# Kernel optimization log

Measured on AMD Instinct MI355X. Metric: run time of the kernel, lower is better.

## Reference

```python
import jax, jax.numpy as jnp
import numpy as np
import math

B, T, D, H = 2, 2048, 1024, 16
DH = D // H          # 64
NB = DH // 2         # 32 rotary pairs
EPS = 1e-5


def setup_inputs() -> dict:
    key = jax.random.key(0)
    ks = jax.random.split(key, 20)
    x = jax.random.normal(ks[0], (B, T, D), dtype=jnp.float32)
    angles = jax.random.uniform(ks[1], (B, H, T, NB), dtype=jnp.float32) * (2.0 * math.pi)
    cos_a = jnp.cos(angles)
    sin_a = jnp.sin(angles)
    sigma = jax.random.uniform(ks[2], (B, T, H, NB), dtype=jnp.float32)
    causal_mask = jnp.triu(jnp.ones((T, T), dtype=bool), k=1)  # True above diag -> masked
    w = lambda k, i, o: jax.random.normal(k, (i, o), dtype=jnp.float32) * 0.02
    return {
        "x": x, "cos_a": cos_a, "sin_a": sin_a, "sigma": sigma, "causal_mask": causal_mask,
        "ln1_g": jnp.ones((D,), jnp.float32), "ln1_b": jnp.zeros((D,), jnp.float32),
        "wq": w(ks[3], D, D), "bq": jnp.zeros((D,), jnp.float32),
        "wk": w(ks[4], D, D), "bk": jnp.zeros((D,), jnp.float32),
        "wv": w(ks[5], D, D), "bv": jnp.zeros((D,), jnp.float32),
        "wo": w(ks[6], D, D), "bo": jnp.zeros((D,), jnp.float32),
        "ln2_g": jnp.ones((D,), jnp.float32), "ln2_b": jnp.zeros((D,), jnp.float32),
        "w1": w(ks[7], D, 4 * D), "b1": jnp.zeros((4 * D,), jnp.float32),
        "w2": w(ks[8], 4 * D, D), "b2": jnp.zeros((D,), jnp.float32),
    }


def _layer_norm(x, g, b):
    mu = jnp.mean(x, axis=-1, keepdims=True)
    var = jnp.mean(jnp.square(x - mu), axis=-1, keepdims=True)
    return (x - mu) * jax.lax.rsqrt(var + EPS) * g + b


def _apply_rope(q, cos_a, sin_a):
    # q: (B,H,T,DH); rotate even/odd pairs by per-pair angles (B,H,T,NB)
    q1 = q[..., 0::2]
    q2 = q[..., 1::2]
    re = q1 * cos_a - q2 * sin_a
    im = q1 * sin_a + q2 * cos_a
    return jnp.stack([re, im], axis=-1).reshape(q.shape)


def reference(x, cos_a, sin_a, sigma, causal_mask,
              ln1_g, ln1_b, wq, bq, wk, bk, wv, bv, wo, bo,
              ln2_g, ln2_b, w1, b1, w2, b2):
    h = _layer_norm(x, ln1_g, ln1_b)
    Q = (h @ wq + bq).reshape(B, T, H, DH).transpose(0, 2, 1, 3)
    K = (h @ wk + bk).reshape(B, T, H, DH).transpose(0, 2, 1, 3)
    V = (h @ wv + bv).reshape(B, T, H, DH).transpose(0, 2, 1, 3)
    Q = _apply_rope(Q, cos_a, sin_a)
    K = _apply_rope(K, cos_a, sin_a)
    # per-(B,H,T) temperature from mean uncertainty
    temp = 1.0 + jnp.mean(sigma, axis=-1).transpose(0, 2, 1)  # (B,H,T)
    scale = math.sqrt(DH)
    scores = jnp.einsum("bhtd,bhsd->bhts", Q, K) / (scale * temp[..., None])
    scores = jnp.where(causal_mask[None, None], -jnp.inf, scores)
    attn = jax.nn.softmax(scores, axis=-1)
    out = jnp.einsum("bhts,bhsd->bhtd", attn, V)
    out = out.transpose(0, 2, 1, 3).reshape(B, T, D)
    x = x + (out @ wo + bo)
    h2 = _layer_norm(x, ln2_g, ln2_b)
    ffn = jax.nn.gelu(h2 @ w1 + b1, approximate=False) @ w2 + b2
    return x + ffn
```

## Files before the change

kernel.cpp:

```cpp
#include <hip/hip_runtime.h>

typedef unsigned short ushort;
typedef unsigned int uint;

typedef __attribute__((ext_vector_type(8))) short short8;
typedef __attribute__((ext_vector_type(8))) unsigned short ushort8;
typedef __attribute__((ext_vector_type(4))) unsigned short ushort4v;
typedef __attribute__((ext_vector_type(4))) float f32x4;
typedef __attribute__((ext_vector_type(4))) uint uint4v;

#define DEV static __device__ __forceinline__

DEV ushort f2b(float f){
  union { float f; uint u; } v; v.f = f;
  uint u = v.u;
  u += 0x7fffu + ((u >> 16) & 1u);
  return (ushort)(u >> 16);
}
DEV float b2f(ushort h){
  union { uint u; float f; } v; v.u = ((uint)h) << 16;
  return v.f;
}
DEV uint cvt_pk_bf16(float lo, float hi){
  uint r;
  asm("v_cvt_pk_bf16_f32 %0, %1, %2" : "=v"(r) : "v"(lo), "v"(hi));
  return r;
}
DEV ushort f2b1(float f){ return (ushort)cvt_pk_bf16(f, f); }
DEV float exp2v(float x){
  float r;
  asm("v_exp_f32 %0, %1" : "=v"(r) : "v"(x));
  return r;
}
DEV float gelu_f(float x){
  float z = fabsf(x) * 0.70710678118654752f;
  float t = __builtin_amdgcn_rcpf(1.f + 0.3275911f * z);
  float poly = t * (0.254829592f + t * (-0.284496736f + t * (1.421413741f +
               t * (-1.453152027f + t * 1.061405429f))));
  float e = exp2v(-z * z * 1.44269504088896f);
  float erf_abs = 1.f - poly * e;
  float erf_s = copysignf(erf_abs, x);
  return 0.5f * x * (1.f + erf_s);
}

constexpr int Bc = 2, Tc = 2048, Dc = 1024, Hc = 16, DHc = 64, NBc = 32;
constexpr int Rc = Bc * Tc;
constexpr int D4c = 4 * Dc;

__global__ __launch_bounds__(256) void k_transcvt(const float* __restrict__ in,
                                                  ushort* __restrict__ out, int K, int N){
  __shared__ float tile[32][33];
  int n0 = blockIdx.x * 32, k0 = blockIdx.y * 32;
  int c = threadIdx.x & 31, r0 = threadIdx.x >> 5;
#pragma unroll
  for (int i = 0; i < 4; i++){
    int k = r0 + i * 8;
    tile[k][c] = in[(size_t)(k0 + k) * N + n0 + c];
  }
  __syncthreads();
#pragma unroll
  for (int i = 0; i < 4; i++){
    int n = r0 + i * 8;
    out[(size_t)(n0 + n) * K + k0 + c] = f2b(tile[c][n]);
  }
}

__global__ __launch_bounds__(256) void k_ln(const float* __restrict__ x, const float* __restrict__ g,
                                            const float* __restrict__ bb, ushort* __restrict__ out){
  int row = blockIdx.x, tid = threadIdx.x;
  const f32x4* xr = (const f32x4*)(x + (size_t)row * Dc);
  f32x4 v = xr[tid];
  float s  = v.x + v.y + v.z + v.w;
  float ss = v.x*v.x + v.y*v.y + v.z*v.z + v.w*v.w;
#pragma unroll
  for (int off = 32; off > 0; off >>= 1){
    s  += __shfl_xor(s,  off, 64);
    ss += __shfl_xor(ss, off, 64);
  }
  __shared__ float red[2][4];
  int w = tid >> 6;
  if ((tid & 63) == 0){ red[0][w] = s; red[1][w] = ss; }
  __syncthreads();
  s  = red[0][0] + red[0][1] + red[0][2] + red[0][3];
  ss = red[1][0] + red[1][1] + red[1][2] + red[1][3];
  float mu  = s * (1.f / Dc);
  float var = ss * (1.f / Dc) - mu * mu;
  float rs  = rsqrtf(var + 1e-5f);
  f32x4 gv = ((const f32x4*)g)[tid];
  f32x4 bv = ((const f32x4*)bb)[tid];
  ushort4v o;
  o.x = f2b((v.x - mu) * rs * gv.x + bv.x);
  o.y = f2b((v.y - mu) * rs * gv.y + bv.y);
  o.z = f2b((v.z - mu) * rs * gv.z + bv.z);
  o.w = f2b((v.w - mu) * rs * gv.w + bv.w);
  ((ushort4v*)(out + (size_t)row * Dc))[tid] = o;
}

#define GLDS(src, dst) __builtin_amdgcn_global_load_lds( \
    (const __attribute__((address_space(1))) void*)(src), \
    (__attribute__((address_space(3))) void*)(dst), 16, 0, 0)

#define STAGE128(nb_, k0_) do { \
  _Pragma("unroll") \
  for (int i_ = 0; i_ < 4; i_++){ \
    int chunk_ = w * 4 + i_; \
    GLDS(A  + (size_t)(m0 + chunk_ * 8 + rloc) * K + (k0_) + gsrc * 8, &SM[nb_][0][chunk_ * 512]); \
    GLDS(Bt + (size_t)(n0 + chunk_ * 8 + rloc) * K + (k0_) + gsrc * 8, &SM[nb_][1][chunk_ * 512]); \
  } \
} while(0)

#define GEMM_CORE(cb_) do { \
  _Pragma("unroll") \
  for (int ks = 0; ks < 2; ks++){ \
    const int gs = (ks * 4 + lg) ^ l7; \
    short8 aF[4], bF[4]; \
    _Pragma("unroll") \
    for (int mi = 0; mi < 4; mi++) aF[mi] = *(const short8*)&SM[cb_][0][(arow + mi * 16) * 64 + gs * 8]; \
    _Pragma("unroll") \
    for (int ni = 0; ni < 4; ni++) bF[ni] = *(const short8*)&SM[cb_][1][(brow + ni * 16) * 64 + gs * 8]; \
    _Pragma("unroll") \
    for (int mi = 0; mi < 4; mi++) \
      _Pragma("unroll") \
      for (int ni = 0; ni < 4; ni++) \
        acc[mi][ni] = __builtin_amdgcn_mfma_f32_16x16x32_bf16(aF[mi], bF[ni], acc[mi][ni], 0, 0, 0); \
  } \
} while(0)

template<int OUT_BF16, int ACT_GELU, int HAS_RES>
__global__ __launch_bounds__(256) void k_gemm(const ushort* __restrict__ A, const ushort* __restrict__ Bt,
                                              const float* __restrict__ bias, const float* __restrict__ resid,
                                              void* __restrict__ Cout, int M, int N, int K){
  __shared__ ushort SM[2][2][8192];
  const int tid = threadIdx.x;
  const int m0 = blockIdx.y * 128, n0 = blockIdx.x * 128;
  const int w = tid >> 6, lane = tid & 63;
  const int wr = w >> 1, wc = w & 1;
  const int la15 = lane & 15, lg = lane >> 4, l7 = lane & 7;
  const int rloc = lane >> 3, gsrc = (lane & 7) ^ rloc;

  f32x4 acc[4][4];
#pragma unroll
  for (int i = 0; i < 4; i++)
#pragma unroll
    for (int j = 0; j < 4; j++) acc[i][j] = f32x4{0.f, 0.f, 0.f, 0.f};

  const int arow = wr * 64 + la15;
  const int brow = wc * 64 + la15;

  STAGE128(0, 0);
  __syncthreads();
  const int NT = K >> 6;
  for (int t = 0; t < NT; t++){
    const int cb = t & 1;
    if (t + 1 < NT) STAGE128(cb ^ 1, (t + 1) << 6);
    GEMM_CORE(cb);
    __syncthreads();
  }

  if (OUT_BF16){
    ushort* Cs = &SM[0][0][0];
#pragma unroll
    for (int mi = 0; mi < 4; mi++)
#pragma unroll
      for (int ni = 0; ni < 4; ni++){
        int ccl = wc * 64 + ni * 16 + la15;
        float bv = bias[n0 + ccl];
        f32x4 a4 = acc[mi][ni];
#pragma unroll
        for (int r = 0; r < 4; r++){
          int rl = wr * 64 + mi * 16 + lg * 4 + r;
          float v = a4[r] + bv;
          if (ACT_GELU) v = gelu_f(v);
          Cs[rl * 136 + ccl] = f2b1(v);
        }
      }
    __syncthreads();
#pragma unroll
    for (int p = 0; p < 8; p++){
      int row = p * 16 + (tid >> 4);
      int col = (tid & 15) * 8;
      ushort8 vv = *(const ushort8*)&Cs[row * 136 + col];
      *(ushort8*)((ushort*)Cout + (size_t)(m0 + row) * N + n0 + col) = vv;
    }
  } else {
#pragma unroll
    for (int mi = 0; mi < 4; mi++)
#pragma unroll
      for (int ni = 0; ni < 4; ni++){
        int cc = n0 + wc * 64 + ni * 16 + la15;
        float bv = bias[cc];
        f32x4 a4 = acc[mi][ni];
#pragma unroll
        for (int r = 0; r < 4; r++){
          int rr = m0 + wr * 64 + mi * 16 + lg * 4 + r;
          float v = a4[r] + bv;
          if (HAS_RES) v += resid[(size_t)rr * N + cc];
          ((float*)Cout)[(size_t)rr * N + cc] = v;
        }
      }
  }
}

__global__ __launch_bounds__(256) void k_gemm_qkv(const ushort* __restrict__ A, const ushort* __restrict__ Bt,
                                                  const float* __restrict__ bq_, const float* __restrict__ bk_,
                                                  const float* __restrict__ bv_, ushort* __restrict__ oq,
                                                  ushort* __restrict__ ok, ushort* __restrict__ ovt, int K){
  __shared__ ushort SM[2][2][8192];
  const int tid = threadIdx.x;
  const int m0 = blockIdx.y * 128, n0 = blockIdx.x * 128;
  const int w = tid >> 6, lane = tid & 63;
  const int wr = w >> 1, wc = w & 1;
  const int la15 = lane & 15, lg = lane >> 4, l7 = lane & 7;
  const int rloc = lane >> 3, gsrc = (lane & 7) ^ rloc;

  f32x4 acc[4][4];
#pragma unroll
  for (int i = 0; i < 4; i++)
#pragma unroll
    for (int j = 0; j < 4; j++) acc[i][j] = f32x4{0.f, 0.f, 0.f, 0.f};

  const int arow = wr * 64 + la15;
  const int brow = wc * 64 + la15;

  STAGE128(0, 0);
  __syncthreads();
  const int NT = K >> 6;
  for (int t = 0; t < NT; t++){
    const int cb = t & 1;
    if (t + 1 < NT) STAGE128(cb ^ 1, (t + 1) << 6);
    GEMM_CORE(cb);
    __syncthreads();
  }

  const int sel = n0 >> 10;
  ushort* Cs = &SM[0][0][0];
  if (sel < 2){
    const float* bias = sel == 0 ? bq_ : bk_;
    ushort* o = sel == 0 ? oq : ok;
#pragma unroll
    for (int mi = 0; mi < 4; mi++)
#pragma unroll
      for (int ni = 0; ni < 4; ni++){
        int ccl = wc * 64 + ni * 16 + la15;
        float bv = bias[(n0 & 1023) + ccl];
        f32x4 a4 = acc[mi][ni];
#pragma unroll
        for (int r = 0; r < 4; r++){
          int rl = wr * 64 + mi * 16 + lg * 4 + r;
          Cs[rl * 136 + ccl] = f2b1(a4[r] + bv);
        }
      }
    __syncthreads();
#pragma unroll
    for (int p = 0; p < 8; p++){
      int row = p * 16 + (tid >> 4);
      int col = (tid & 15) * 8;
      ushort8 vv = *(const ushort8*)&Cs[row * 136 + col];
      *(ushort8*)(o + (size_t)(m0 + row) * Dc + (n0 & 1023) + col) = vv;
    }
  } else {
#pragma unroll
    for (int mi = 0; mi < 4; mi++)
#pragma unroll
      for (int ni = 0; ni < 4; ni++){
        int ccl = wc * 64 + ni * 16 + la15;
        float bv = bv_[(n0 - 2048) + ccl];
        f32x4 a4 = acc[mi][ni];
#pragma unroll
        for (int r = 0; r < 4; r++){
          int rl = wr * 64 + mi * 16 + lg * 4 + r;
          Cs[ccl * 136 + rl] = f2b1(a4[r] + bv);
        }
      }
    __syncthreads();
    const int bb = m0 >> 11, t0 = m0 & 2047;
#pragma unroll
    for (int p = 0; p < 8; p++){
      int nl = p * 16 + (tid >> 4);
      int tl = (tid & 15) * 8;
      ushort8 vv = *(const ushort8*)&Cs[nl * 136 + tl];
      int ng = (n0 - 2048) + nl;
      *(ushort8*)(ovt + ((size_t)(bb * 1024 + ng) << 11) + t0 + tl) = vv;
    }
  }
}

__global__ __launch_bounds__(256) void k_rope(ushort* __restrict__ q, ushort* __restrict__ k,
                                              const float* __restrict__ ca, const float* __restrict__ sa){
  int idx = blockIdx.x * 256 + threadIdx.x;
  int nb = idx & 31;
  int hh = (idx >> 5) & 15;
  int t  = (idx >> 9) & 2047;
  int b  = idx >> 20;
  size_t base = (size_t)(b * Tc + t) * Dc + hh * DHc + nb * 2;
  int ai = ((b * Hc + hh) * Tc + t) * NBc + nb;
  float c = ca[ai], s = sa[ai];
  uint qu = *(const uint*)(q + base);
  float q1 = b2f((ushort)(qu & 0xffff)), q2 = b2f((ushort)(qu >> 16));
  *(uint*)(q + base) = cvt_pk_bf16(q1 * c - q2 * s, q1 * s + q2 * c);
  uint ku = *(const uint*)(k + base);
  float k1 = b2f((ushort)(ku & 0xffff)), k2 = b2f((ushort)(ku >> 16));
  *(uint*)(k + base) = cvt_pk_bf16(k1 * c - k2 * s, k1 * s + k2 * c);
}

__global__ __launch_bounds__(256) void k_iscale(const float* __restrict__ sigma, float* __restrict__ isc){
  int idx = blockIdx.x * 256 + threadIdx.x;
  int hh = idx & 15;
  int t  = (idx >> 4) & 2047;
  int b  = idx >> 15;
  const f32x4* sp = (const f32x4*)(sigma + (size_t)idx * NBc);
  float s = 0.f;
#pragma unroll
  for (int i = 0; i < 8; i++){ f32x4 v = sp[i]; s += v.x + v.y + v.z + v.w; }
  isc[(b * Hc + hh) * Tc + t] = 1.44269504088896f / (8.f * (1.f + s * (1.f / NBc)));
}

__global__ __launch_bounds__(64) void k_attn_mfma(const ushort* __restrict__ qb, const ushort* __restrict__ kb,
                                                  const ushort* __restrict__ vtb, const float* __restrict__ isc,
                                                  ushort* __restrict__ ao){
  __shared__ ushort smem[8192];
  const int bid = blockIdx.x;
  const int bh = bid & 31, b = bh >> 4, h = bh & 15;
  const int qt = 63 - (bid >> 5);
  const int lane = threadIdx.x;
  const int la15 = lane & 15, lg = lane >> 4, l7 = lane & 7;
  const int q0w = qt * 32;

  short8 qf[2][2];
  float iscv[2];
#pragma unroll
  for (int sub = 0; sub < 2; sub++){
    int qg = q0w + sub * 16 + la15;
    size_t rb = (size_t)(b * Tc + qg) * Dc + h * DHc;
    qf[sub][0] = *(const short8*)(qb + rb + lg * 8);
    qf[sub][1] = *(const short8*)(qb + rb + 32 + lg * 8);
    iscv[sub] = isc[bh * Tc + qg];
  }

  f32x4 O[2][4];
#pragma unroll
  for (int sub = 0; sub < 2; sub++)
#pragma unroll
    for (int dt = 0; dt < 4; dt++) O[sub][dt] = f32x4{0.f, 0.f, 0.f, 0.f};
  float lacc[2] = {0.f, 0.f};

  const ushort* kbase  = kb + (size_t)b * Tc * Dc + h * DHc;
  const ushort* vtbase = vtb + (size_t)bh * DHc * Tc;
  const int ktmax = q0w + 31;

  const int Rl = lane >> 3, sl = lane & 7;
  const int gK = sl ^ ((Rl & 3) ^ (((Rl >> 3) & 3) << 1));
  const int gV = sl ^ (Rl & 7);

#define STAGE_KV(kt_) do { \
  _Pragma("unroll") \
  for (int i_ = 0; i_ < 8; i_++){ \
    int R_ = i_ * 8 + Rl; \
    int gk_ = sl ^ ((R_ & 3) ^ (((R_ >> 3) & 3) << 1)); \
    GLDS(kbase + (size_t)((kt_) + R_) * Dc + gk_ * 8, &smem[i_ * 512]); \
    GLDS(vtbase + (size_t)R_ * Tc + (kt_) + gV * 8, &smem[4096 + i_ * 512]); \
  } \
} while(0)

#define COMPUTE_T(kt_) do { \
  _Pragma("unroll") \
  for (int sub = 0; sub < 2; sub++){ \
    f32x4 s_[4]; \
    __builtin_amdgcn_s_setprio(1); \
    _Pragma("unroll") \
    for (int t_ = 0; t_ < 4; t_++){ \
      s_[t_] = f32x4{0.f, 0.f, 0.f, 0.f}; \
      s_[t_] = __builtin_amdgcn_mfma_f32_16x16x32_bf16(kf[t_][0], qf[sub][0], s_[t_], 0, 0, 0); \
      s_[t_] = __builtin_amdgcn_mfma_f32_16x16x32_bf16(kf[t_][1], qf[sub][1], s_[t_], 0, 0, 0); \
    } \
    __builtin_amdgcn_s_setprio(0); \
    const int qg_ = q0w + sub * 16 + la15; \
    const float sc_ = iscv[sub]; \
    const bool diag_ = ((kt_) + 63 > q0w + sub * 16); \
    uint up_[4][2]; \
    float lp_ = 0.f; \
    _Pragma("unroll") \
    for (int t_ = 0; t_ < 4; t_++){ \
      _Pragma("unroll") \
      for (int pr_ = 0; pr_ < 2; pr_++){ \
        float e0_ = exp2v(s_[t_][2 * pr_] * sc_); \
        float e1_ = exp2v(s_[t_][2 * pr_ + 1] * sc_); \
        if (diag_){ \
          int kp0_ = (kt_) + ((t_ >> 1) << 5) + lg * 8 + ((t_ & 1) << 2) + 2 * pr_; \
          if (kp0_ > qg_)     e0_ = 0.f; \
          if (kp0_ + 1 > qg_) e1_ = 0.f; \
        } \
        lp_ += e0_ + e1_; \
        up_[t_][pr_] = cvt_pk_bf16(e0_, e1_); \
      } \
    } \
    lacc[sub] += lp_; \
    __builtin_amdgcn_s_setprio(1); \
    _Pragma("unroll") \
    for (int kh_ = 0; kh_ < 2; kh_++){ \
      union { uint4v w; short8 s8; } pfr_; \
      pfr_.w[0] = up_[kh_ * 2][0];     pfr_.w[1] = up_[kh_ * 2][1]; \
      pfr_.w[2] = up_[kh_ * 2 + 1][0]; pfr_.w[3] = up_[kh_ * 2 + 1][1]; \
      _Pragma("unroll") \
      for (int dt_ = 0; dt_ < 4; dt_++) \
        O[sub][dt_] = __builtin_amdgcn_mfma_f32_16x16x32_bf16(vtf[dt_][kh_], pfr_.s8, O[sub][dt_], 0, 0, 0); \
    } \
    __builtin_amdgcn_s_setprio(0); \
  } \
} while(0)

  STAGE_KV(0);
  asm volatile("s_waitcnt vmcnt(0)" ::: "memory");
  __builtin_amdgcn_sched_barrier(0);

  const int swzr = (la15 & 3) ^ ((la15 >> 2) << 1);
  for (int kt = 0;; kt += 64){
    short8 kf[4][2], vtf[4][2];
#pragma unroll
    for (int t_ = 0; t_ < 4; t_++){
      int r = ((t_ >> 1) << 5) + ((la15 >> 2) << 3) + ((t_ & 1) << 2) + (la15 & 3);
#pragma unroll
      for (int ds = 0; ds < 2; ds++){
        int g = (ds * 4 + lg) ^ swzr;
        kf[t_][ds] = *(const short8*)&smem[r * 64 + g * 8];
      }
    }
#pragma unroll
    for (int dt = 0; dt < 4; dt++){
      int d = dt * 16 + la15;
#pragma unroll
      for (int kh = 0; kh < 2; kh++){
        int g = (kh * 4 + lg) ^ (la15 & 7);
        vtf[dt][kh] = *(const short8*)&smem[4096 + d * 64 + g * 8];
      }
    }
    asm volatile("s_waitcnt lgkmcnt(0)" ::: "memory");
    __builtin_amdgcn_sched_barrier(0);
    STAGE_KV(kt + 64);
    COMPUTE_T(kt);
    if (kt + 64 > ktmax) break;
    asm volatile("s_waitcnt vmcnt(0)" ::: "memory");
    __builtin_amdgcn_sched_barrier(0);
  }
  asm volatile("s_waitcnt vmcnt(0)" ::: "memory");
  __builtin_amdgcn_sched_barrier(0);

  char* osb = (char*)smem;
#pragma unroll
  for (int sub = 0; sub < 2; sub++){
    float lt = lacc[sub];
    lt += __shfl_xor(lt, 16, 64);
    lt += __shfl_xor(lt, 32, 64);
    float inv = 1.f / lt;
#pragma unroll
    for (int dt = 0; dt < 4; dt++)
#pragma unroll
      for (int pr = 0; pr < 2; pr++){
        uint u = cvt_pk_bf16(O[sub][dt][2 * pr] * inv, O[sub][dt][2 * pr + 1] * inv);
        *(uint*)(osb + (sub * 16 + la15) * 136 + (dt * 16 + lg * 4 + pr * 2) * 2) = u;
      }
  }
#pragma unroll
  for (int it = 0; it < 4; it++){
    int ql = it * 8 + (lane >> 3);
    ushort8 v = *(const ushort8*)(osb + ql * 136 + l7 * 16);
    *(ushort8*)(ao + (size_t)(b * Tc + q0w + ql) * Dc + h * DHc + l7 * 8) = v;
  }
}

extern "C" void kernel_launch(void* const* d_in, const int* in_sizes, int n_in,
                              void* d_out, int out_size, void* d_ws, size_t ws_size,
                              hipStream_t stream){
  (void)in_sizes; (void)n_in; (void)out_size; (void)ws_size;
  const float* x    = (const float*)d_in[0];
  const float* cosa = (const float*)d_in[1];
  const float* sina = (const float*)d_in[2];
  const float* sigma= (const float*)d_in[3];
  const float* ln1g = (const float*)d_in[5];
  const float* ln1b = (const float*)d_in[6];
  const float* wq   = (const float*)d_in[7];
  const float* bq   = (const float*)d_in[8];
  const float* wk   = (const float*)d_in[9];
  const float* bk   = (const float*)d_in[10];
  const float* wv   = (const float*)d_in[11];
  const float* bv   = (const float*)d_in[12];
  const float* wo   = (const float*)d_in[13];
  const float* bo   = (const float*)d_in[14];
  const float* ln2g = (const float*)d_in[15];
  const float* ln2b = (const float*)d_in[16];
  const float* w1   = (const float*)d_in[17];
  const float* b1   = (const float*)d_in[18];
  const float* w2   = (const float*)d_in[19];
  const float* b2   = (const float*)d_in[20];
  float* out = (float*)d_out;

  char* ws = (char*)d_ws;
  constexpr size_t MB = 1024 * 1024;
  ushort* wqT  = (ushort*)(ws +  0 * MB);
  ushort* wkT  = (ushort*)(ws +  2 * MB);
  ushort* wvT  = (ushort*)(ws +  4 * MB);
  ushort* woT  = (ushort*)(ws +  6 * MB);
  ushort* w1T  = (ushort*)(ws +  8 * MB);
  ushort* w2T  = (ushort*)(ws + 16 * MB);
  ushort* hb   = (ushort*)(ws + 24 * MB);
  ushort* qbuf = (ushort*)(ws + 32 * MB);
  ushort* kbuf = (ushort*)(ws + 40 * MB);
  ushort* vtb  = (ushort*)(ws + 48 * MB);
  ushort* aob  = (ushort*)(ws + 56 * MB);
  float*  x2   = (float*)(ws + 64 * MB);
  float*  iscp = (float*)(ws + 80 * MB);
  ushort* g1b  = qbuf;

  k_transcvt<<<dim3(Dc / 32, Dc / 32), 256, 0, stream>>>(wq, wqT, Dc, Dc);
  k_transcvt<<<dim3(Dc / 32, Dc / 32), 256, 0, stream>>>(wk, wkT, Dc, Dc);
  k_transcvt<<<dim3(Dc / 32, Dc / 32), 256, 0, stream>>>(wv, wvT, Dc, Dc);
  k_transcvt<<<dim3(Dc / 32, Dc / 32), 256, 0, stream>>>(wo, woT, Dc, Dc);
  k_transcvt<<<dim3(D4c / 32, Dc / 32), 256, 0, stream>>>(w1, w1T, Dc, D4c);
  k_transcvt<<<dim3(Dc / 32, D4c / 32), 256, 0, stream>>>(w2, w2T, D4c, Dc);
  k_ln<<<Rc, 256, 0, stream>>>(x, ln1g, ln1b, hb);
  k_gemm_qkv<<<dim3(3 * Dc / 128, Rc / 128), 256, 0, stream>>>(hb, wqT, bq, bk, bv, qbuf, kbuf, vtb, Dc);
  k_rope<<<(Bc * Tc * Hc * NBc) / 256, 256, 0, stream>>>(qbuf, kbuf, cosa, sina);
  k_iscale<<<(Bc * Tc * Hc) / 256, 256, 0, stream>>>(sigma, iscp);
  k_attn_mfma<<<dim3(2048), 64, 0, stream>>>(qbuf, kbuf, vtb, iscp, aob);
  k_gemm<0, 0, 1><<<dim3(Dc / 128, Rc / 128), 256, 0, stream>>>(aob, woT, bo, x, x2, Rc, Dc, Dc);
  k_ln<<<Rc, 256, 0, stream>>>(x2, ln2g, ln2b, hb);
  k_gemm<1, 1, 0><<<dim3(D4c / 128, Rc / 128), 256, 0, stream>>>(hb, w1T, b1, nullptr, g1b, Rc, D4c, Dc);
  k_gemm<0, 0, 1><<<dim3(Dc / 128, Rc / 128), 256, 0, stream>>>(g1b, w2T, b2, x2, out, Rc, Dc, D4c);
}
```

Baseline: 248.1 us.

## Use 256x256-tile multi-stage pipelined GEMM for QKV and FFN1 projections

Adds a templated 512-thread GEMM kernel with 256x256 output tiles and 128 KB of dynamic LDS. It streams 32-wide K chunks through a three-slot pipeline, interleaving explicit waitcnt/barrier steps with MFMA blocks. It replaces the 128x128 QKV GEMM and the GELU FFN1 GEMM, aiming for more data reuse per loaded tile and fewer blocks. The trade-off is far fewer workgroups (192 and 256) on a 256-CU part, so some CUs may sit idle, plus a two-pass epilogue through LDS.

```diff
diff --git a/kernel.cpp b/kernel.cpp
--- a/kernel.cpp
+++ b/kernel.cpp
@@ -201,86 +201,172 @@
   }
 }
 
-__global__ __launch_bounds__(256) void k_gemm_qkv(const ushort* __restrict__ A, const ushort* __restrict__ Bt,
-                                                  const float* __restrict__ bq_, const float* __restrict__ bk_,
-                                                  const float* __restrict__ bv_, ushort* __restrict__ oq,
-                                                  ushort* __restrict__ ok, ushort* __restrict__ ovt, int K){
-  __shared__ ushort SM[2][2][8192];
+#define ST_HALF(dstU, P, base_, kc_) do{ \
+  _Pragma("unroll") \
+  for (int j_ = 0; j_ < 2; j_++){ \
+    int c_ = w * 2 + j_; \
+    GLDS(P + (size_t)((base_) + c_ * 16 + (lane >> 2)) * K + (kc_) + (lane & 3) * 8, &SM[(dstU) + c_ * 512]); \
+  } }while(0)
+
+#define RD_A(s_, ch_, mh_) do{ \
+  const ushort* Aarr_ = &SM[(s_) * 32768 + (ch_) * 8192]; \
+  int ab_ = (wr * 128 + (mh_) * 64 + la15) * 32 + lg4 * 8; \
+  _Pragma("unroll") \
+  for (int q_ = 0; q_ < 4; q_++) aF[q_] = *(const short8*)&Aarr_[ab_ + q_ * 512]; }while(0)
+
+#define RD_B(s_, ch_) do{ \
+  const ushort* Barr_ = &SM[(s_) * 32768 + 16384 + (ch_) * 8192]; \
+  int bb_ = (wc * 64 + la15) * 32 + lg4 * 8; \
+  _Pragma("unroll") \
+  for (int q_ = 0; q_ < 4; q_++) bF[q_] = *(const short8*)&Barr_[bb_ + q_ * 512]; }while(0)
+
+#define MM16(mh_) do{ __builtin_amdgcn_s_setprio(1); \
+  _Pragma("unroll") \
+  for (int m_ = 0; m_ < 4; m_++) \
+    _Pragma("unroll") \
+    for (int n_ = 0; n_ < 4; n_++) \
+      acc[(mh_) * 4 + m_][n_] = __builtin_amdgcn_mfma_f32_16x16x32_bf16(aF[m_], bF[n_], acc[(mh_) * 4 + m_][n_], 0, 0, 0); \
+  __builtin_amdgcn_s_setprio(0); }while(0)
+
+#define LGKM0 asm volatile("s_waitcnt lgkmcnt(0)" ::: "memory")
+#define VM8   asm volatile("s_waitcnt vmcnt(8)" ::: "memory")
+#define BARR  __builtin_amdgcn_s_barrier()
+
+template<int QKV, int GELU>
+__global__ __launch_bounds__(512, 2) void k_g256(const ushort* __restrict__ A, const ushort* __restrict__ Bt,
+                                                 const float* __restrict__ b0, const float* __restrict__ b1_,
+                                                 const float* __restrict__ b2_, ushort* __restrict__ o0,
+                                                 ushort* __restrict__ o1, ushort* __restrict__ ovt,
+                                                 int N, int K){
+  extern __shared__ ushort SM[];
   const int tid = threadIdx.x;
-  const int m0 = blockIdx.y * 128, n0 = blockIdx.x * 128;
   const int w = tid >> 6, lane = tid & 63;
-  const int wr = w >> 1, wc = w & 1;
-  const int la15 = lane & 15, lg = lane >> 4, l7 = lane & 7;
-  const int rloc = lane >> 3, gsrc = (lane & 7) ^ rloc;
-
-  f32x4 acc[4][4];
-#pragma unroll
-  for (int i = 0; i < 4; i++)
+  const int wr = w >> 2, wc = w & 3;
+  const int la15 = lane & 15, lg4 = lane >> 4;
+  const int m0 = blockIdx.y * 256, n0 = blockIdx.x * 256;
+
+  f32x4 acc[8][4];
+#pragma unroll
+  for (int i = 0; i < 8; i++)
 #pragma unroll
     for (int j = 0; j < 4; j++) acc[i][j] = f32x4{0.f, 0.f, 0.f, 0.f};
-
-  const int arow = wr * 64 + la15;
-  const int brow = wc * 64 + la15;
-
-  STAGE128(0, 0);
+  short8 aF[4], bF[4];
+
+  ST_HALF(0,             A,  m0, 0);
+  ST_HALF(16384,         Bt, n0, 0);
+  ST_HALF(8192,          A,  m0, 32);
+  ST_HALF(24576,         Bt, n0, 32);
+  ST_HALF(32768,         A,  m0, 64);
+  ST_HALF(32768 + 16384, Bt, n0, 64);
+  VM8; BARR;
+
+  const int NP = K >> 7;
+  for (int i = 0; i < NP; i++){
+    const int kb = i << 7;
+    RD_A(0, 0, 0); RD_B(0, 0); LGKM0; ST_HALF(32768 + 8192,  A,  m0, kb + 96);       BARR; MM16(0);
+    RD_A(0, 0, 1);             LGKM0; ST_HALF(32768 + 24576, Bt, n0, kb + 96);  VM8; BARR; MM16(1);
+    RD_A(0, 1, 0); RD_B(0, 1); LGKM0; ST_HALF(0,             A,  m0, kb + 128);      BARR; MM16(0);
+    RD_A(0, 1, 1);             LGKM0; ST_HALF(16384,         Bt, n0, kb + 128); VM8; BARR; MM16(1);
+    RD_A(1, 0, 0); RD_B(1, 0); LGKM0; ST_HALF(8192,          A,  m0, kb + 160);      BARR; MM16(0);
+    RD_A(1, 0, 1);             LGKM0; ST_HALF(24576,         Bt, n0, kb + 160); VM8; BARR; MM16(1);
+    RD_A(1, 1, 0); RD_B(1, 1); LGKM0; ST_HALF(32768,         A,  m0, kb + 192);      BARR; MM16(0);
+    RD_A(1, 1, 1);             LGKM0; ST_HALF(32768 + 16384, Bt, n0, kb + 192); VM8; BARR; MM16(1);
+  }
+  asm volatile("s_waitcnt vmcnt(0)" ::: "memory");
   __syncthreads();
-  const int NT = K >> 6;
-  for (int t = 0; t < NT; t++){
-    const int cb = t & 1;
-    if (t + 1 < NT) STAGE128(cb ^ 1, (t + 1) << 6);
-    GEMM_CORE(cb);
-    __syncthreads();
-  }
-
-  const int sel = n0 >> 10;
-  ushort* Cs = &SM[0][0][0];
-  if (sel < 2){
-    const float* bias = sel == 0 ? bq_ : bk_;
-    ushort* o = sel == 0 ? oq : ok;
-#pragma unroll
-    for (int mi = 0; mi < 4; mi++)
-#pragma unroll
-      for (int ni = 0; ni < 4; ni++){
-        int ccl = wc * 64 + ni * 16 + la15;
-        float bv = bias[(n0 & 1023) + ccl];
-        f32x4 a4 = acc[mi][ni];
-#pragma unroll
-        for (int r = 0; r < 4; r++){
-          int rl = wr * 64 + mi * 16 + lg * 4 + r;
-          Cs[rl * 136 + ccl] = f2b1(a4[r] + bv);
-        }
-      }
-    __syncthreads();
-#pragma unroll
-    for (int p = 0; p < 8; p++){
-      int row = p * 16 + (tid >> 4);
-      int col = (tid & 15) * 8;
-      ushort8 vv = *(const ushort8*)&Cs[row * 136 + col];
-      *(ushort8*)(o + (size_t)(m0 + row) * Dc + (n0 & 1023) + col) = vv;
+
+  if (QKV == 0){
+#pragma unroll
+    for (int h = 0; h < 2; h++){
+      if (wr == h){
+#pragma unroll
+        for (int MI = 0; MI < 8; MI++)
+#pragma unroll
+          for (int ni = 0; ni < 4; ni++){
+            int ccl = wc * 64 + ni * 16 + la15;
+            float bv = b0[n0 + ccl];
+            f32x4 a4 = acc[MI][ni];
+#pragma unroll
+            for (int r = 0; r < 4; r++){
+              int rl = MI * 16 + lg4 * 4 + r;
+              float v = a4[r] + bv;
+              if (GELU) v = gelu_f(v);
+              SM[rl * 264 + ccl] = f2b1(v);
+            }
+          }
+      }
+      __syncthreads();
+#pragma unroll
+      for (int it = 0; it < 8; it++){
+        int row = it * 16 + (tid >> 5);
+        int col = (tid & 31) * 8;
+        ushort8 vv = *(const ushort8*)&SM[row * 264 + col];
+        *(ushort8*)(o0 + (size_t)(m0 + h * 128 + row) * N + n0 + col) = vv;
+      }
+      __syncthreads();
     }
   } else {
-#pragma unroll
-    for (int mi = 0; mi < 4; mi++)
-#pragma unroll
-      for (int ni = 0; ni < 4; ni++){
-        int ccl = wc * 64 + ni * 16 + la15;
-        float bv = bv_[(n0 - 2048) + ccl];
-        f32x4 a4 = acc[mi][ni];
-#pragma unroll
-        for (int r = 0; r < 4; r++){
-          int rl = wr * 64 + mi * 16 + lg * 4 + r;
-          Cs[ccl * 136 + rl] = f2b1(a4[r] + bv);
+    const int sel = n0 >> 10;
+    if (sel < 2){
+      const float* bias = sel == 0 ? b0 : b1_;
+      ushort* o = sel == 0 ? o0 : o1;
+#pragma unroll
+      for (int h = 0; h < 2; h++){
+        if (wr == h){
+#pragma unroll
+          for (int MI = 0; MI < 8; MI++)
+#pragma unroll
+            for (int ni = 0; ni < 4; ni++){
+              int ccl = wc * 64 + ni * 16 + la15;
+              float bv = bias[(n0 & 1023) + ccl];
+              f32x4 a4 = acc[MI][ni];
+#pragma unroll
+              for (int r = 0; r < 4; r++){
+                int rl = MI * 16 + lg4 * 4 + r;
+                SM[rl * 264 + ccl] = f2b1(a4[r] + bv);
+              }
+            }
         }
-      }
-    __syncthreads();
-    const int bb = m0 >> 11, t0 = m0 & 2047;
-#pragma unroll
-    for (int p = 0; p < 8; p++){
-      int nl = p * 16 + (tid >> 4);
-      int tl = (tid & 15) * 8;
-      ushort8 vv = *(const ushort8*)&Cs[nl * 136 + tl];
-      int ng = (n0 - 2048) + nl;
-      *(ushort8*)(ovt + ((size_t)(bb * 1024 + ng) << 11) + t0 + tl) = vv;
+        __syncthreads();
+#pragma unroll
+        for (int it = 0; it < 8; it++){
+          int row = it * 16 + (tid >> 5);
+          int col = (tid & 31) * 8;
+          ushort8 vv = *(const ushort8*)&SM[row * 264 + col];
+          *(ushort8*)(o + (size_t)(m0 + h * 128 + row) * Dc + (n0 & 1023) + col) = vv;
+        }
+        __syncthreads();
+      }
+    } else {
+      const int bb = m0 >> 11, t0 = m0 & 2047;
+#pragma unroll
+      for (int h = 0; h < 2; h++){
+        if (wr == h){
+#pragma unroll
+          for (int MI = 0; MI < 8; MI++)
+#pragma unroll
+            for (int ni = 0; ni < 4; ni++){
+              int ccl = wc * 64 + ni * 16 + la15;
+              float bv = b2_[(n0 - 2048) + ccl];
+              f32x4 a4 = acc[MI][ni];
+#pragma unroll
+              for (int r = 0; r < 4; r++){
+                int rl = MI * 16 + lg4 * 4 + r;
+                SM[ccl * 136 + rl] = f2b1(a4[r] + bv);
+              }
+            }
+        }
+        __syncthreads();
+#pragma unroll
+        for (int it = 0; it < 8; it++){
+          int nl = it * 32 + (tid >> 4);
+          int tl = (tid & 15) * 8;
+          ushort8 vv = *(const ushort8*)&SM[nl * 136 + tl];
+          int ng = (n0 - 2048) + nl;
+          *(ushort8*)(ovt + ((size_t)(bb * 1024 + ng) << 11) + t0 + h * 128 + tl) = vv;
+        }
+        __syncthreads();
+      }
     }
   }
 }
@@ -349,7 +435,6 @@
   const int ktmax = q0w + 31;
 
   const int Rl = lane >> 3, sl = lane & 7;
-  const int gK = sl ^ ((Rl & 3) ^ (((Rl >> 3) & 3) << 1));
   const int gV = sl ^ (Rl & 7);
 
 #define STAGE_KV(kt_) do { \
@@ -413,7 +498,6 @@
   asm volatile("s_waitcnt vmcnt(0)" ::: "memory");
   __builtin_amdgcn_sched_barrier(0);
 
-  const int swzr = (la15 & 3) ^ ((la15 >> 2) << 1);
   for (int kt = 0;; kt += 64){
     short8 kf[4][2], vtf[4][2];
 #pragma unroll
@@ -421,7 +505,7 @@
       int r = ((t_ >> 1) << 5) + ((la15 >> 2) << 3) + ((t_ & 1) << 2) + (la15 & 3);
 #pragma unroll
       for (int ds = 0; ds < 2; ds++){
-        int g = (ds * 4 + lg) ^ swzr;
+        int g = (ds * 4 + lg) ^ ((la15 & 3) ^ ((la15 >> 2) << 1));
         kf[t_][ds] = *(const short8*)&smem[r * 64 + g * 8];
       }
     }
@@ -518,12 +602,14 @@
   k_transcvt<<<dim3(D4c / 32, Dc / 32), 256, 0, stream>>>(w1, w1T, Dc, D4c);
   k_transcvt<<<dim3(Dc / 32, D4c / 32), 256, 0, stream>>>(w2, w2T, D4c, Dc);
   k_ln<<<Rc, 256, 0, stream>>>(x, ln1g, ln1b, hb);
-  k_gemm_qkv<<<dim3(3 * Dc / 128, Rc / 128), 256, 0, stream>>>(hb, wqT, bq, bk, bv, qbuf, kbuf, vtb, Dc);
+  k_g256<1, 0><<<dim3(3 * Dc / 256, Rc / 256), 512, 131072, stream>>>(
+      hb, wqT, bq, bk, bv, qbuf, kbuf, vtb, Dc, Dc);
   k_rope<<<(Bc * Tc * Hc * NBc) / 256, 256, 0, stream>>>(qbuf, kbuf, cosa, sina);
   k_iscale<<<(Bc * Tc * Hc) / 256, 256, 0, stream>>>(sigma, iscp);
   k_attn_mfma<<<dim3(2048), 64, 0, stream>>>(qbuf, kbuf, vtb, iscp, aob);
   k_gemm<0, 0, 1><<<dim3(Dc / 128, Rc / 128), 256, 0, stream>>>(aob, woT, bo, x, x2, Rc, Dc, Dc);
   k_ln<<<Rc, 256, 0, stream>>>(x2, ln2g, ln2b, hb);
-  k_gemm<1, 1, 0><<<dim3(D4c / 128, Rc / 128), 256, 0, stream>>>(hb, w1T, b1, nullptr, g1b, Rc, D4c, Dc);
+  k_g256<0, 1><<<dim3(D4c / 256, Rc / 256), 512, 131072, stream>>>(
+      hb, w1T, b1, nullptr, nullptr, g1b, nullptr, nullptr, D4c, Dc);
   k_gemm<0, 0, 1><<<dim3(Dc / 128, Rc / 128), 256, 0, stream>>>(g1b, w2T, b2, x2, out, Rc, Dc, D4c);
 }
```

After: 254.2 us. 2.5% more time.
